# Kernel optimization log

Measured on AMD Instinct MI355X. Metric: run time of the kernel, lower is better.

Reference implementation:

```python
import jax, jax.numpy as jnp
import numpy as np

DIM = 128
CODEBOOK_SIZE = 1024


def setup_inputs() -> dict:
    key = jax.random.key(0)
    kx, ke = jax.random.split(key)
    x = jax.random.normal(kx, (64, 1500, DIM), dtype=jnp.float32)
    # uniform_init uses kaiming_uniform_ on [K, D]: U(-b, b), b = sqrt(6 / fan_in) with a=sqrt(5) -> gain adjusts bound
    bound = float(np.sqrt(1.0 / DIM))  # kaiming_uniform with a=sqrt(5): bound = sqrt(6/((1+5)*fan_in)) = sqrt(1/fan_in)
    embed = jax.random.uniform(ke, (CODEBOOK_SIZE, DIM), dtype=jnp.float32, minval=-bound, maxval=bound)
    return {"x": x, "embed": embed}


def reference(x, embed):
    # x: [B, T, D], embed: [K, D]
    B, T, D = x.shape
    flat = x.reshape(-1, D)  # [N, D]
    dist = (2.0 * (flat @ embed.T)
            - jnp.sum(flat * flat, axis=-1, keepdims=True)
            - jnp.sum(embed * embed, axis=-1))  # [N, K]
    embed_ind = jnp.argmax(dist, axis=-1).reshape(B, T)  # [B, T]
    quantize = embed[embed_ind]  # [B, T, D] gather
    return quantize, embed_ind
```

## Files before the change

kernel.cpp:

```cpp
#include <hip/hip_runtime.h>
#include <hip/hip_fp16.h>

#define DIM 128
#define KCODES 1024
#define BROWS 128
#define NCH (KCODES / 16)
#define TAU_ACC 1.2e-3f

typedef _Float16 f16x8 __attribute__((ext_vector_type(8)));
typedef float f32x4 __attribute__((ext_vector_type(4)));

__global__ void enorm_kernel(const float* __restrict__ embed, float* __restrict__ enorm) {
    int k = blockIdx.x * blockDim.x + threadIdx.x;
    if (k < KCODES) {
        const float4* row = (const float4*)(embed + (size_t)k * DIM);
        float s = 0.f;
#pragma unroll
        for (int d = 0; d < DIM / 4; ++d) {
            float4 v = row[d];
            s = fmaf(v.x, v.x, s); s = fmaf(v.y, v.y, s);
            s = fmaf(v.z, v.z, s); s = fmaf(v.w, v.w, s);
        }
        enorm[k] = s;
    }
}

__global__ void pack_kernel(const float* __restrict__ embed, _Float16* __restrict__ Ehp) {
    int t = blockIdx.x * blockDim.x + threadIdx.x;
    int n  = t & 15;
    int q  = (t >> 4) & 3;
    int ks = (t >> 6) & 3;
    int c  = t >> 8;
    const float* src = embed + (size_t)(c * 16 + n) * DIM + ks * 32 + q * 8;
    float4 a0 = *(const float4*)src;
    float4 a1 = *(const float4*)(src + 4);
    float f[8] = {a0.x, a0.y, a0.z, a0.w, a1.x, a1.y, a1.z, a1.w};
    f16x8 h8;
#pragma unroll
    for (int j = 0; j < 8; ++j) h8[j] = (_Float16)f[j];
    *(f16x8*)&Ehp[(size_t)t * 8] = h8;
}

__global__ __launch_bounds__(256, 3)
void argmax_mfma_kernel(const float* __restrict__ x, const float* __restrict__ embed,
                        const _Float16* __restrict__ Ehp, const float* __restrict__ enorm,
                        float* __restrict__ outq, float* __restrict__ outi) {
    __shared__ float enorm_l[KCODES];
    __shared__ int idx_l[BROWS];
    __shared__ int flist[BROWS];
    __shared__ float rbest[4];
    __shared__ int   rbidx[4];
    __shared__ int fcnt;

    const int tid  = threadIdx.x;
    const int w    = tid >> 6;
    const int lane = tid & 63;
    const int n    = lane & 15;
    const int q    = lane >> 4;
    const size_t row0 = (size_t)blockIdx.x * BROWS;

    if (tid == 0) fcnt = 0;
    {
        float4 e4 = ((const float4*)enorm)[tid];
        float4 v; v.x = -0.5f * e4.x; v.y = -0.5f * e4.y; v.z = -0.5f * e4.z; v.w = -0.5f * e4.w;
        ((float4*)enorm_l)[tid] = v;
    }

    const _Float16* EhpL = Ehp + (size_t)lane * 8;
    f16x8 bA0, bA1, bA2, bA3, bB0, bB1, bB2, bB3;
#define LOADB(P, B0, B1, B2, B3) do {                  \
    const _Float16* p_ = (P);                          \
    B0 = *(const f16x8*)(p_);                          \
    B1 = *(const f16x8*)(p_ + 512);                    \
    B2 = *(const f16x8*)(p_ + 1024);                   \
    B3 = *(const f16x8*)(p_ + 1536); } while (0)

    LOADB(EhpL, bA0, bA1, bA2, bA3);
    LOADB(EhpL + 2048, bB0, bB1, bB2, bB3);

    f16x8 xh[2][4], xl[2][4];
#pragma unroll
    for (int s = 0; s < 2; ++s)
#pragma unroll
        for (int ks = 0; ks < 4; ++ks) {
            const float* xp = x + (row0 + (size_t)(w * 32 + s * 16 + n)) * DIM + ks * 32 + q * 8;
            float4 a0 = *(const float4*)xp;
            float4 a1 = *(const float4*)(xp + 4);
            float f[8] = {a0.x, a0.y, a0.z, a0.w, a1.x, a1.y, a1.z, a1.w};
            f16x8 h, l;
#pragma unroll
            for (int j = 0; j < 8; ++j) {
                _Float16 hh = (_Float16)f[j];
                h[j] = hh;
                l[j] = (_Float16)(f[j] - (float)hh);
            }
            xh[s][ks] = h; xl[s][ks] = l;
        }

    __syncthreads();

    float best[2][4], sec[2][4]; int bidx[2][4];
#pragma unroll
    for (int s = 0; s < 2; ++s)
#pragma unroll
        for (int rg = 0; rg < 4; ++rg) { best[s][rg] = -3.4e38f; sec[s][rg] = -3.4e38f; bidx[s][rg] = 0; }

#define PROC(CI, B0, B1, B2, B3, EV) do {                                             \
    const int code_ = (CI) * 16 + n;                                                  \
    f32x4 h0 = {EV, EV, EV, EV}, l0 = {0.f, 0.f, 0.f, 0.f};                           \
    f32x4 h1 = {EV, EV, EV, EV}, l1 = {0.f, 0.f, 0.f, 0.f};                           \
    h0 = __builtin_amdgcn_mfma_f32_16x16x32_f16(xh[0][0], B0, h0, 0, 0, 0);           \
    h1 = __builtin_amdgcn_mfma_f32_16x16x32_f16(xh[1][0], B0, h1, 0, 0, 0);           \
    l0 = __builtin_amdgcn_mfma_f32_16x16x32_f16(xl[0][0], B0, l0, 0, 0, 0);           \
    l1 = __builtin_amdgcn_mfma_f32_16x16x32_f16(xl[1][0], B0, l1, 0, 0, 0);           \
    h0 = __builtin_amdgcn_mfma_f32_16x16x32_f16(xh[0][1], B1, h0, 0, 0, 0);           \
    h1 = __builtin_amdgcn_mfma_f32_16x16x32_f16(xh[1][1], B1, h1, 0, 0, 0);           \
    l0 = __builtin_amdgcn_mfma_f32_16x16x32_f16(xl[0][1], B1, l0, 0, 0, 0);           \
    l1 = __builtin_amdgcn_mfma_f32_16x16x32_f16(xl[1][1], B1, l1, 0, 0, 0);           \
    h0 = __builtin_amdgcn_mfma_f32_16x16x32_f16(xh[0][2], B2, h0, 0, 0, 0);           \
    h1 = __builtin_amdgcn_mfma_f32_16x16x32_f16(xh[1][2], B2, h1, 0, 0, 0);           \
    l0 = __builtin_amdgcn_mfma_f32_16x16x32_f16(xl[0][2], B2, l0, 0, 0, 0);           \
    l1 = __builtin_amdgcn_mfma_f32_16x16x32_f16(xl[1][2], B2, l1, 0, 0, 0);           \
    h0 = __builtin_amdgcn_mfma_f32_16x16x32_f16(xh[0][3], B3, h0, 0, 0, 0);           \
    h1 = __builtin_amdgcn_mfma_f32_16x16x32_f16(xh[1][3], B3, h1, 0, 0, 0);           \
    l0 = __builtin_amdgcn_mfma_f32_16x16x32_f16(xl[0][3], B3, l0, 0, 0, 0);           \
    l1 = __builtin_amdgcn_mfma_f32_16x16x32_f16(xl[1][3], B3, l1, 0, 0, 0);           \
    _Pragma("unroll")                                                                 \
    for (int rg = 0; rg < 4; ++rg) {                                                  \
        float sc0 = h0[rg] + l0[rg];                                                  \
        sec[0][rg]  = __builtin_amdgcn_fmed3f(best[0][rg], sec[0][rg], sc0);          \
        bidx[0][rg] = (sc0 > best[0][rg]) ? code_ : bidx[0][rg];                      \
        best[0][rg] = fmaxf(best[0][rg], sc0);                                        \
        float sc1 = h1[rg] + l1[rg];                                                  \
        sec[1][rg]  = __builtin_amdgcn_fmed3f(best[1][rg], sec[1][rg], sc1);          \
        bidx[1][rg] = (sc1 > best[1][rg]) ? code_ : bidx[1][rg];                      \
        best[1][rg] = fmaxf(best[1][rg], sc1);                                        \
    }                                                                                 \
} while (0)

    float eA = enorm_l[0 * 16 + n];
    float eB = enorm_l[1 * 16 + n];
#pragma unroll 1
    for (int cc = 0; cc < NCH; cc += 2) {
        float eA2 = enorm_l[((cc + 2) & (NCH - 1)) * 16 + n];
        float eB2 = enorm_l[((cc + 3) & (NCH - 1)) * 16 + n];
        const _Float16* p2 = EhpL + (size_t)((cc + 2) & (NCH - 1)) * 2048;
        const _Float16* p3 = EhpL + (size_t)((cc + 3) & (NCH - 1)) * 2048;
        PROC(cc, bA0, bA1, bA2, bA3, eA);
        LOADB(p2, bA0, bA1, bA2, bA3);
        PROC(cc + 1, bB0, bB1, bB2, bB3, eB);
        LOADB(p3, bB0, bB1, bB2, bB3);
        eA = eA2; eB = eB2;
    }
#undef PROC
#undef LOADB

#pragma unroll
    for (int mask = 1; mask < 16; mask <<= 1) {
#pragma unroll
        for (int s = 0; s < 2; ++s)
#pragma unroll
            for (int rg = 0; rg < 4; ++rg) {
                float ob = __shfl_xor(best[s][rg], mask);
                float os = __shfl_xor(sec[s][rg], mask);
                int   oi = __shfl_xor(bidx[s][rg], mask);
                if (ob > best[s][rg] || (ob == best[s][rg] && oi < bidx[s][rg])) {
                    sec[s][rg] = fmaxf(best[s][rg], os);
                    best[s][rg] = ob; bidx[s][rg] = oi;
                } else {
                    sec[s][rg] = fmaxf(sec[s][rg], ob);
                }
            }
    }
    if (n == 0) {
#pragma unroll
        for (int s = 0; s < 2; ++s)
#pragma unroll
            for (int rg = 0; rg < 4; ++rg) {
                int r = w * 32 + s * 16 + q * 4 + rg;
                idx_l[r] = bidx[s][rg];
                if (best[s][rg] - sec[s][rg] < TAU_ACC) {
                    int p = atomicAdd(&fcnt, 1);
                    flist[p] = r;
                }
            }
    }
    __syncthreads();

    int nf = fcnt;
    for (int f = 0; f < nf; ++f) {
        int r = flist[f];
        const float4* xg4 = (const float4*)(x + (row0 + r) * DIM);
        float b = -3.4e38f; int bi = 0;
        int cbase = w * 256 + lane * 4;
        for (int c = cbase; c < cbase + 4; ++c) {
            const float4* eg4 = (const float4*)(embed + (size_t)c * DIM);
            float s = 0.f;
#pragma unroll 8
            for (int d = 0; d < DIM / 4; ++d) {
                float4 xv = xg4[d], ev = eg4[d];
                s = fmaf(xv.x, ev.x, s); s = fmaf(xv.y, ev.y, s);
                s = fmaf(xv.z, ev.z, s); s = fmaf(xv.w, ev.w, s);
            }
            float sc = fmaf(2.f, s, -enorm[c]);
            if (sc > b) { b = sc; bi = c; }
        }
#pragma unroll
        for (int mask = 1; mask < 64; mask <<= 1) {
            float ob = __shfl_xor(b, mask);
            int   oi = __shfl_xor(bi, mask);
            if (ob > b || (ob == b && oi < bi)) { b = ob; bi = oi; }
        }
        if (lane == 0) { rbest[w] = b; rbidx[w] = bi; }
        __syncthreads();
        if (tid == 0) {
            float B = rbest[0]; int BI = rbidx[0];
#pragma unroll
            for (int i = 1; i < 4; ++i)
                if (rbest[i] > B || (rbest[i] == B && rbidx[i] < BI)) { B = rbest[i]; BI = rbidx[i]; }
            idx_l[r] = BI;
        }
        __syncthreads();
    }
    __syncthreads();

    const float4* e4 = (const float4*)embed;
    float4* oq4 = (float4*)outq + row0 * (DIM / 4);
#pragma unroll
    for (int i = 0; i < 16; ++i) {
        int g = tid + i * 256;
        int r = g >> 5, d4 = g & 31;
        int id = idx_l[r];
        oq4[g] = e4[(size_t)id * (DIM / 4) + d4];
    }
    if (tid < BROWS) outi[row0 + tid] = (float)idx_l[tid];
}

extern "C" void kernel_launch(void* const* d_in, const int* in_sizes, int n_in,
                              void* d_out, int out_size, void* d_ws, size_t ws_size,
                              hipStream_t stream) {
    const float* x     = (const float*)d_in[0];
    const float* embed = (const float*)d_in[1];
    const int x_elems  = in_sizes[0];
    const int n_rows   = x_elems / DIM;

    float*    enorm = (float*)d_ws;
    _Float16* Ehp   = (_Float16*)((char*)d_ws + 4096);

    float* outq = (float*)d_out;
    float* outi = (float*)d_out + (size_t)x_elems;

    enorm_kernel<<<KCODES / 256, 256, 0, stream>>>(embed, enorm);
    pack_kernel<<<KCODES * 16 / 256, 256, 0, stream>>>(embed, Ehp);
    argmax_mfma_kernel<<<n_rows / BROWS, 256, 0, stream>>>(x, embed, Ehp, enorm, outq, outi);
}
```

Measured before the change: 242.0 us.

## Stage codebook chunks in LDS with double-buffered global_load_lds

```diff
diff --git a/kernel.cpp b/kernel.cpp
--- a/kernel.cpp
+++ b/kernel.cpp
@@ -4,11 +4,19 @@
 #define DIM 128
 #define KCODES 1024
 #define BROWS 128
-#define NCH (KCODES / 16)
+#define CCHUNK 64
+#define NCHUNKS (KCODES / CCHUNK)
+#define CH_HALFS (CCHUNK * DIM)
 #define TAU_ACC 1.2e-3f
 
 typedef _Float16 f16x8 __attribute__((ext_vector_type(8)));
 typedef float f32x4 __attribute__((ext_vector_type(4)));
+
+__device__ __forceinline__ void gl_lds16(const void* g, void* l) {
+    __builtin_amdgcn_global_load_lds(
+        (const __attribute__((address_space(1))) void*)g,
+        (__attribute__((address_space(3))) void*)l, 16, 0, 0);
+}
 
 __global__ void enorm_kernel(const float* __restrict__ embed, float* __restrict__ enorm) {
     int k = blockIdx.x * blockDim.x + threadIdx.x;
@@ -45,6 +53,7 @@
 void argmax_mfma_kernel(const float* __restrict__ x, const float* __restrict__ embed,
                         const _Float16* __restrict__ Ehp, const float* __restrict__ enorm,
                         float* __restrict__ outq, float* __restrict__ outi) {
+    __shared__ __align__(16) _Float16 ebuf[2][CH_HALFS];
     __shared__ float enorm_l[KCODES];
     __shared__ int idx_l[BROWS];
     __shared__ int flist[BROWS];
@@ -66,17 +75,13 @@
         ((float4*)enorm_l)[tid] = v;
     }
 
-    const _Float16* EhpL = Ehp + (size_t)lane * 8;
-    f16x8 bA0, bA1, bA2, bA3, bB0, bB1, bB2, bB3;
-#define LOADB(P, B0, B1, B2, B3) do {                  \
-    const _Float16* p_ = (P);                          \
-    B0 = *(const f16x8*)(p_);                          \
-    B1 = *(const f16x8*)(p_ + 512);                    \
-    B2 = *(const f16x8*)(p_ + 1024);                   \
-    B3 = *(const f16x8*)(p_ + 1536); } while (0)
-
-    LOADB(EhpL, bA0, bA1, bA2, bA3);
-    LOADB(EhpL + 2048, bB0, bB1, bB2, bB3);
+    {
+        const _Float16* gsrc = Ehp + (size_t)w * 2048 + (size_t)lane * 8;
+        _Float16* ldst = &ebuf[0][w * 2048];
+#pragma unroll
+        for (int ks = 0; ks < 4; ++ks)
+            gl_lds16(gsrc + ks * 512, ldst + ks * 512);
+    }
 
     f16x8 xh[2][4], xl[2][4];
 #pragma unroll
@@ -105,8 +110,13 @@
 #pragma unroll
         for (int rg = 0; rg < 4; ++rg) { best[s][rg] = -3.4e38f; sec[s][rg] = -3.4e38f; bidx[s][rg] = 0; }
 
-#define PROC(CI, B0, B1, B2, B3, EV) do {                                             \
+#define PROC(CI, EBC, EV) do {                                                        \
     const int code_ = (CI) * 16 + n;                                                  \
+    const _Float16* ebc_ = (EBC) + (size_t)lane * 8;                                  \
+    f16x8 B0 = *(const f16x8*)(ebc_);                                                 \
+    f16x8 B1 = *(const f16x8*)(ebc_ + 512);                                           \
+    f16x8 B2 = *(const f16x8*)(ebc_ + 1024);                                          \
+    f16x8 B3 = *(const f16x8*)(ebc_ + 1536);                                          \
     f32x4 h0 = {EV, EV, EV, EV}, l0 = {0.f, 0.f, 0.f, 0.f};                           \
     f32x4 h1 = {EV, EV, EV, EV}, l1 = {0.f, 0.f, 0.f, 0.f};                           \
     h0 = __builtin_amdgcn_mfma_f32_16x16x32_f16(xh[0][0], B0, h0, 0, 0, 0);           \
@@ -138,22 +148,30 @@
     }                                                                                 \
 } while (0)
 
-    float eA = enorm_l[0 * 16 + n];
-    float eB = enorm_l[1 * 16 + n];
+    int curb = 0;
 #pragma unroll 1
-    for (int cc = 0; cc < NCH; cc += 2) {
-        float eA2 = enorm_l[((cc + 2) & (NCH - 1)) * 16 + n];
-        float eB2 = enorm_l[((cc + 3) & (NCH - 1)) * 16 + n];
-        const _Float16* p2 = EhpL + (size_t)((cc + 2) & (NCH - 1)) * 2048;
-        const _Float16* p3 = EhpL + (size_t)((cc + 3) & (NCH - 1)) * 2048;
-        PROC(cc, bA0, bA1, bA2, bA3, eA);
-        LOADB(p2, bA0, bA1, bA2, bA3);
-        PROC(cc + 1, bB0, bB1, bB2, bB3, eB);
-        LOADB(p3, bB0, bB1, bB2, bB3);
-        eA = eA2; eB = eB2;
+    for (int kt = 0; kt < NCHUNKS; ++kt) {
+        if (kt + 1 < NCHUNKS) {
+            const _Float16* gsrc = Ehp + (size_t)(kt + 1) * CH_HALFS
+                                       + (size_t)w * 2048 + (size_t)lane * 8;
+            _Float16* ldst = &ebuf[curb ^ 1][w * 2048];
+#pragma unroll
+            for (int ks = 0; ks < 4; ++ks)
+                gl_lds16(gsrc + ks * 512, ldst + ks * 512);
+        }
+        const _Float16* eb = &ebuf[curb][0];
+        float e0 = enorm_l[kt * 64 + n];
+        float e1 = enorm_l[kt * 64 + 16 + n];
+        float e2 = enorm_l[kt * 64 + 32 + n];
+        float e3 = enorm_l[kt * 64 + 48 + n];
+        PROC(kt * 4 + 0, eb, e0);
+        PROC(kt * 4 + 1, eb + 2048, e1);
+        PROC(kt * 4 + 2, eb + 4096, e2);
+        PROC(kt * 4 + 3, eb + 6144, e3);
+        __syncthreads();
+        curb ^= 1;
     }
 #undef PROC
-#undef LOADB
 
 #pragma unroll
     for (int mask = 1; mask < 16; mask <<= 1) {
```

New measurement: 243.8 us. About the same (+0.7%).

## Split fp32 refinement and gather into separate kernels with global flag list

Applied to the files above, without the earlier changes.

```diff
diff --git a/kernel.cpp b/kernel.cpp
--- a/kernel.cpp
+++ b/kernel.cpp
@@ -10,8 +10,10 @@
 typedef _Float16 f16x8 __attribute__((ext_vector_type(8)));
 typedef float f32x4 __attribute__((ext_vector_type(4)));
 
-__global__ void enorm_kernel(const float* __restrict__ embed, float* __restrict__ enorm) {
+__global__ void enorm_kernel(const float* __restrict__ embed, float* __restrict__ enorm,
+                             int* __restrict__ fcnt_g) {
     int k = blockIdx.x * blockDim.x + threadIdx.x;
+    if (k == 0) *fcnt_g = 0;
     if (k < KCODES) {
         const float4* row = (const float4*)(embed + (size_t)k * DIM);
         float s = 0.f;
@@ -42,15 +44,11 @@
 }
 
 __global__ __launch_bounds__(256, 3)
-void argmax_mfma_kernel(const float* __restrict__ x, const float* __restrict__ embed,
+void argmax_mfma_kernel(const float* __restrict__ x,
                         const _Float16* __restrict__ Ehp, const float* __restrict__ enorm,
-                        float* __restrict__ outq, float* __restrict__ outi) {
+                        float* __restrict__ outi, int* __restrict__ fcnt_g,
+                        int* __restrict__ flags) {
     __shared__ float enorm_l[KCODES];
-    __shared__ int idx_l[BROWS];
-    __shared__ int flist[BROWS];
-    __shared__ float rbest[4];
-    __shared__ int   rbidx[4];
-    __shared__ int fcnt;
 
     const int tid  = threadIdx.x;
     const int w    = tid >> 6;
@@ -59,7 +57,6 @@
     const int q    = lane >> 4;
     const size_t row0 = (size_t)blockIdx.x * BROWS;
 
-    if (tid == 0) fcnt = 0;
     {
         float4 e4 = ((const float4*)enorm)[tid];
         float4 v; v.x = -0.5f * e4.x; v.y = -0.5f * e4.y; v.z = -0.5f * e4.z; v.w = -0.5f * e4.w;
@@ -177,22 +174,31 @@
         for (int s = 0; s < 2; ++s)
 #pragma unroll
             for (int rg = 0; rg < 4; ++rg) {
-                int r = w * 32 + s * 16 + q * 4 + rg;
-                idx_l[r] = bidx[s][rg];
+                int R = (int)row0 + w * 32 + s * 16 + q * 4 + rg;
+                outi[R] = (float)bidx[s][rg];
                 if (best[s][rg] - sec[s][rg] < TAU_ACC) {
-                    int p = atomicAdd(&fcnt, 1);
-                    flist[p] = r;
+                    int p = atomicAdd(fcnt_g, 1);
+                    flags[p] = R;
                 }
             }
     }
-    __syncthreads();
-
-    int nf = fcnt;
-    for (int f = 0; f < nf; ++f) {
-        int r = flist[f];
-        const float4* xg4 = (const float4*)(x + (row0 + r) * DIM);
+}
+
+__global__ __launch_bounds__(256, 4)
+void refine_kernel(const float* __restrict__ x, const float* __restrict__ embed,
+                   const float* __restrict__ enorm, const int* __restrict__ fcnt_g,
+                   const int* __restrict__ flags, float* __restrict__ outi) {
+    __shared__ float rbest[4];
+    __shared__ int   rbidx[4];
+    const int tid  = threadIdx.x;
+    const int w    = tid >> 6;
+    const int lane = tid & 63;
+    const int nf = *fcnt_g;
+    for (int f = blockIdx.x; f < nf; f += gridDim.x) {
+        int R = flags[f];
+        const float4* xg4 = (const float4*)(x + (size_t)R * DIM);
         float b = -3.4e38f; int bi = 0;
-        int cbase = w * 256 + lane * 4;
+        int cbase = tid * 4;
         for (int c = cbase; c < cbase + 4; ++c) {
             const float4* eg4 = (const float4*)(embed + (size_t)c * DIM);
             float s = 0.f;
@@ -218,22 +224,19 @@
 #pragma unroll
             for (int i = 1; i < 4; ++i)
                 if (rbest[i] > B || (rbest[i] == B && rbidx[i] < BI)) { B = rbest[i]; BI = rbidx[i]; }
-            idx_l[r] = BI;
+            outi[R] = (float)BI;
         }
         __syncthreads();
     }
-    __syncthreads();
-
-    const float4* e4 = (const float4*)embed;
-    float4* oq4 = (float4*)outq + row0 * (DIM / 4);
-#pragma unroll
-    for (int i = 0; i < 16; ++i) {
-        int g = tid + i * 256;
-        int r = g >> 5, d4 = g & 31;
-        int id = idx_l[r];
-        oq4[g] = e4[(size_t)id * (DIM / 4) + d4];
-    }
-    if (tid < BROWS) outi[row0 + tid] = (float)idx_l[tid];
+}
+
+__global__ __launch_bounds__(256, 8)
+void gather_kernel(const float* __restrict__ embed, const float* __restrict__ outi,
+                   float* __restrict__ outq) {
+    int g = blockIdx.x * 256 + threadIdx.x;
+    int r = g >> 5, d4 = g & 31;
+    int id = (int)outi[r];
+    ((float4*)outq)[g] = ((const float4*)embed)[(size_t)id * (DIM / 4) + d4];
 }
 
 extern "C" void kernel_launch(void* const* d_in, const int* in_sizes, int n_in,
@@ -245,12 +248,16 @@
     const int n_rows   = x_elems / DIM;
 
     float*    enorm = (float*)d_ws;
-    _Float16* Ehp   = (_Float16*)((char*)d_ws + 4096);
+    int*      fcnt  = (int*)((char*)d_ws + 4096);
+    int*      flags = (int*)((char*)d_ws + 8192);
+    _Float16* Ehp   = (_Float16*)((char*)d_ws + 8192 + n_rows * 4);
 
     float* outq = (float*)d_out;
     float* outi = (float*)d_out + (size_t)x_elems;
 
-    enorm_kernel<<<KCODES / 256, 256, 0, stream>>>(embed, enorm);
+    enorm_kernel<<<KCODES / 256, 256, 0, stream>>>(embed, enorm, fcnt);
     pack_kernel<<<KCODES * 16 / 256, 256, 0, stream>>>(embed, Ehp);
-    argmax_mfma_kernel<<<n_rows / BROWS, 256, 0, stream>>>(x, embed, Ehp, enorm, outq, outi);
-}
+    argmax_mfma_kernel<<<n_rows / BROWS, 256, 0, stream>>>(x, Ehp, enorm, outi, fcnt, flags);
+    refine_kernel<<<2048, 256, 0, stream>>>(x, embed, enorm, fcnt, flags, outi);
+    gather_kernel<<<n_rows * (DIM / 4) / 256, 256, 0, stream>>>(embed, outi, outq);
+}
```

Result: faster. 198.2 us (-18.1%).
